# Optimization experiments

Measured on AMD Instinct MI355X. Metric: run time of the kernel, lower is better.

Reference implementation:

```python
import jax, jax.numpy as jnp
import numpy as np

N_NODES = 10000
N_EDGES = 160000
IN_DIM = 512
HID = 256
HEADS = 4
OUT_DIM = 512
NEG_SLOPE = 0.2  # PyG GATConv default


def _glorot(key, shape):
    fan_in, fan_out = shape[0], shape[-1]
    lim = jnp.sqrt(6.0 / (fan_in + fan_out))
    return jax.random.uniform(key, shape, jnp.float32, -lim, lim)


def setup_inputs() -> dict:
    key = jax.random.key(0)
    ks = jax.random.split(key, 16)
    x = jax.random.normal(ks[0], (N_NODES, IN_DIM), jnp.float32)
    edge_index = jax.random.randint(ks[1], (2, N_EDGES), 0, N_NODES, jnp.int64)
    # layer 1: GATConv(512 -> 256, heads=4, concat) -> out 1024
    W1 = _glorot(ks[2], (IN_DIM, HEADS * HID))
    att_src1 = _glorot(ks[3], (HEADS, HID))
    att_dst1 = _glorot(ks[4], (HEADS, HID))
    b1 = jnp.zeros((HEADS * HID,), jnp.float32)
    # layer 2: GATConv(1024 -> 256, heads=4, concat) -> out 1024
    W2 = _glorot(ks[5], (HEADS * HID, HEADS * HID))
    att_src2 = _glorot(ks[6], (HEADS, HID))
    att_dst2 = _glorot(ks[7], (HEADS, HID))
    b2 = jnp.zeros((HEADS * HID,), jnp.float32)
    # final fc: 1024 -> 512
    fcW = _glorot(ks[8], (HEADS * HID, OUT_DIM))
    fcb = jnp.zeros((OUT_DIM,), jnp.float32)
    return dict(x=x, edge_index=edge_index, W1=W1, att_src1=att_src1,
                att_dst1=att_dst1, b1=b1, W2=W2, att_src2=att_src2,
                att_dst2=att_dst2, b2=b2, fcW=fcW, fcb=fcb)


def gat_conv(x, src, dst, W, att_src, att_dst, bias):
    # x: [N, F_in]; src/dst: [E] (self-loops already included)
    N = x.shape[0]
    h = (x @ W).reshape(N, HEADS, HID)                       # [N, H, C]
    a_src = jnp.sum(h * att_src, axis=-1)                    # [N, H]
    a_dst = jnp.sum(h * att_dst, axis=-1)                    # [N, H]
    e = jax.nn.leaky_relu(a_src[src] + a_dst[dst], NEG_SLOPE)  # [E, H]
    # numerically stable segment softmax over destination nodes
    m = jax.ops.segment_max(e, dst, num_segments=N)          # [N, H]
    e = jnp.exp(e - m[dst])
    s = jax.ops.segment_sum(e, dst, num_segments=N)          # [N, H]
    alpha = e / (s[dst] + 1e-16)                             # [E, H]
    msg = alpha[:, :, None] * h[src]                         # [E, H, C]
    out = jax.ops.segment_sum(msg, dst, num_segments=N)      # [N, H, C]
    return out.reshape(N, HEADS * HID) + bias


def reference(x, edge_index, W1, att_src1, att_dst1, b1,
              W2, att_src2, att_dst2, b2, fcW, fcb):
    N = x.shape[0]
    loops = jnp.arange(N, dtype=edge_index.dtype)
    src = jnp.concatenate([edge_index[0], loops])  # PyG add_self_loops=True
    dst = jnp.concatenate([edge_index[1], loops])
    h = gat_conv(x, src, dst, W1, att_src1, att_dst1, b1)
    h = jax.nn.relu(h)  # dropout is identity in eval mode
    h = gat_conv(h, src, dst, W2, att_src2, att_dst2, b2)
    h = jax.nn.relu(h)
    return h @ fcW + fcb
```

## Files before the change

kernel.cpp:

```cpp
#include <hip/hip_runtime.h>
#include <hip/hip_bf16.h>

#define NN 10000
#define NE 160000
#define NET 170000
#define IN_DIM 512
#define D1 1024
#define HEADS 4
#define HID 256
#define OUT_DIM 512
#define NEG_SLOPE 0.2f

typedef __attribute__((ext_vector_type(8))) short bf16x8;
typedef __attribute__((ext_vector_type(4))) float f32x4;

__device__ inline float b2f(unsigned short b) {
    union { unsigned u; float f; } x; x.u = ((unsigned)b) << 16; return x.f;
}
__device__ inline unsigned short f2b(float f) {
    union { float f; unsigned u; } x; x.f = f;
    unsigned u = x.u;
    unsigned r = u + 0x7FFFu + ((u >> 16) & 1u);
    return (unsigned short)(r >> 16);
}
__device__ inline float lrelu(float v) { return v > 0.f ? v : NEG_SLOPE * v; }

__global__ void init_kernel(const int* ei32, int* flag, int* counts, int* cursor) {
    int i = blockIdx.x * blockDim.x + threadIdx.x;
    if (i < NN) { counts[i] = 0; cursor[i] = 0; }
    if (blockIdx.x == 0) {
        __shared__ int nz;
        if (threadIdx.x == 0) nz = 0;
        __syncthreads();
        int acc = 0;
        for (int k = threadIdx.x; k < 500; k += 256) acc |= ei32[2 * k + 1];
        if (acc) atomicOr(&nz, 1);
        __syncthreads();
        if (threadIdx.x == 0) flag[0] = (nz == 0) ? 1 : 0;
    }
}

__device__ inline void load_edge(const void* ei, int f64, int e, int& s, int& d) {
    if (f64) {
        const long long* p = (const long long*)ei;
        s = (int)p[e]; d = (int)p[NE + e];
    } else {
        const int* p = (const int*)ei;
        s = p[e]; d = p[NE + e];
    }
}

__global__ void count_kernel(const void* ei, const int* flag, int* counts) {
    int e = blockIdx.x * blockDim.x + threadIdx.x;
    if (e >= NET) return;
    int s, d;
    if (e < NE) load_edge(ei, *flag, e, s, d);
    else d = e - NE;
    atomicAdd(&counts[d], 1);
}

__global__ __launch_bounds__(256) void scan_kernel(const int* counts, int* indptr) {
    __shared__ int part[256];
    int t = threadIdx.x;
    int base = t * 40;
    int local[40];
    int sum = 0;
#pragma unroll
    for (int k = 0; k < 40; k++) {
        int i = base + k;
        int c = (i < NN) ? counts[i] : 0;
        local[k] = sum;
        sum += c;
    }
    part[t] = sum;
    __syncthreads();
    for (int off = 1; off < 256; off <<= 1) {
        int v = (t >= off) ? part[t - off] : 0;
        __syncthreads();
        part[t] += v;
        __syncthreads();
    }
    int excl = part[t] - sum;
#pragma unroll
    for (int k = 0; k < 40; k++) {
        int i = base + k;
        if (i < NN) indptr[i] = excl + local[k];
    }
    if (t == 255) indptr[NN] = part[255];
}

__global__ void fill_kernel(const void* ei, const int* flag, const int* indptr,
                            int* cursor, int* csr_src) {
    int e = blockIdx.x * blockDim.x + threadIdx.x;
    if (e >= NET) return;
    int s, d;
    if (e < NE) load_edge(ei, *flag, e, s, d);
    else { s = e - NE; d = s; }
    int pos = indptr[d] + atomicAdd(&cursor[d], 1);
    csr_src[pos] = s;
}

__device__ void tpose_tile(const float* __restrict__ in, unsigned short* __restrict__ out,
                           int R, int C, int bx, int by) {
    __shared__ float tile[32][33];
    int tx = threadIdx.x & 31, ty = threadIdx.x >> 5;
    int c = bx * 32 + tx;
#pragma unroll
    for (int r0 = 0; r0 < 32; r0 += 8) {
        int r = by * 32 + ty + r0;
        tile[ty + r0][tx] = in[(size_t)r * C + c];
    }
    __syncthreads();
    int oc = by * 32 + tx;
#pragma unroll
    for (int r0 = 0; r0 < 32; r0 += 8) {
        int orow = bx * 32 + ty + r0;
        out[(size_t)orow * R + oc] = f2b(tile[tx][ty + r0]);
    }
}

#define CVT_NB 5000
#define TP1_NB 512
#define TP2_NB 1024
#define TP3_NB 512
__global__ __launch_bounds__(256) void prep_kernel(
    const float* __restrict__ x, unsigned short* __restrict__ xb,
    const float* __restrict__ W1, unsigned short* __restrict__ W1t,
    const float* __restrict__ W2, unsigned short* __restrict__ W2t,
    const float* __restrict__ fcW, unsigned short* __restrict__ fcWt) {
    int b = blockIdx.x;
    if (b < CVT_NB) {
        int i = b * 256 + threadIdx.x;
        float4 v = reinterpret_cast<const float4*>(x)[i];
        ushort4 o;
        o.x = f2b(v.x); o.y = f2b(v.y); o.z = f2b(v.z); o.w = f2b(v.w);
        reinterpret_cast<ushort4*>(xb)[i] = o;
        return;
    }
    b -= CVT_NB;
    if (b < TP1_NB) { tpose_tile(W1, W1t, IN_DIM, D1, b & 31, b >> 5); return; }
    b -= TP1_NB;
    if (b < TP2_NB) { tpose_tile(W2, W2t, D1, D1, b & 31, b >> 5); return; }
    b -= TP2_NB;
    tpose_tile(fcW, fcWt, D1, OUT_DIM, b & 15, b >> 4);
}

#define BM 128
#define BN 128
#define BK 64
__global__ __launch_bounds__(256) void gemm128(
    const unsigned short* __restrict__ A, const unsigned short* __restrict__ B,
    const float* __restrict__ bias, float* __restrict__ Cf, unsigned short* __restrict__ Cb,
    int M, int N, int K, int NB) {
    __shared__ __align__(16) unsigned short As[BM * BK];
    __shared__ __align__(16) unsigned short Bs[BN * BK];
    int t = threadIdx.x;
    int nwg = gridDim.x;
    int q = nwg >> 3, r = nwg & 7;
    int xcd = blockIdx.x & 7, jj = blockIdx.x >> 3;
    int wg = (xcd < r ? xcd * (q + 1) : r * (q + 1) + (xcd - r) * q) + jj;
    int row0 = (wg / NB) * BM, col0 = (wg % NB) * BN;

    int w = t >> 6, l = t & 63;
    int wr = w >> 1, wc = w & 1;
    f32x4 acc[4][4] = {};

    int srow = w * 8 + (l >> 3);
    int scs = (((l & 7) ^ (l >> 3)) * 8);
    const unsigned short* ap0 = A + (size_t)min(row0 +  0 + srow, M - 1) * K + scs;
    const unsigned short* ap1 = A + (size_t)min(row0 + 32 + srow, M - 1) * K + scs;
    const unsigned short* ap2 = A + (size_t)min(row0 + 64 + srow, M - 1) * K + scs;
    const unsigned short* ap3 = A + (size_t)min(row0 + 96 + srow, M - 1) * K + scs;
    const unsigned short* bp0 = B + (size_t)(col0 +  0 + srow) * K + scs;
    const unsigned short* bp1 = B + (size_t)(col0 + 32 + srow) * K + scs;
    const unsigned short* bp2 = B + (size_t)(col0 + 64 + srow) * K + scs;
    const unsigned short* bp3 = B + (size_t)(col0 + 96 + srow) * K + scs;
    unsigned short* asd0 = As + 0 * 2048 + w * 512;
    unsigned short* asd1 = As + 1 * 2048 + w * 512;
    unsigned short* asd2 = As + 2 * 2048 + w * 512;
    unsigned short* asd3 = As + 3 * 2048 + w * 512;
    unsigned short* bsd0 = Bs + 0 * 2048 + w * 512;
    unsigned short* bsd1 = Bs + 1 * 2048 + w * 512;
    unsigned short* bsd2 = Bs + 2 * 2048 + w * 512;
    unsigned short* bsd3 = Bs + 3 * 2048 + w * 512;

    int rr = l & 15;
    int rb = (rr & 7) << 4;
    int kb0 = (l >> 4) << 4;
    const char* Ab = (const char*)As;
    const char* Bb = (const char*)Bs;

#define GLD(src, dst) __builtin_amdgcn_global_load_lds( \
        (const __attribute__((address_space(1))) void*)(src), \
        (__attribute__((address_space(3))) void*)(dst), 16, 0, 0)

    for (int k0 = 0; k0 < K; k0 += BK) {
        GLD(ap0, asd0); GLD(ap1, asd1); GLD(ap2, asd2); GLD(ap3, asd3);
        GLD(bp0, bsd0); GLD(bp1, bsd1); GLD(bp2, bsd2); GLD(bp3, bsd3);
        ap0 += BK; ap1 += BK; ap2 += BK; ap3 += BK;
        bp0 += BK; bp1 += BK; bp2 += BK; bp3 += BK;
        __syncthreads();

#pragma unroll
        for (int ks = 0; ks < 2; ks++) {
            int kb = ((ks << 6) | kb0) ^ rb;
            bf16x8 af[4], bfv[4];
#pragma unroll
            for (int mi = 0; mi < 4; mi++)
                af[mi] = *reinterpret_cast<const bf16x8*>(
                    Ab + (wr * 64 + mi * 16 + rr) * 128 + kb);
#pragma unroll
            for (int ni = 0; ni < 4; ni++)
                bfv[ni] = *reinterpret_cast<const bf16x8*>(
                    Bb + (wc * 64 + ni * 16 + rr) * 128 + kb);
#pragma unroll
            for (int mi = 0; mi < 4; mi++)
#pragma unroll
                for (int ni = 0; ni < 4; ni++)
                    acc[mi][ni] = __builtin_amdgcn_mfma_f32_16x16x32_bf16(
                        af[mi], bfv[ni], acc[mi][ni], 0, 0, 0);
        }
        __syncthreads();
    }
#undef GLD

    int c_l = l & 15, r_h = (l >> 4) * 4;
#pragma unroll
    for (int mi = 0; mi < 4; mi++)
#pragma unroll
        for (int ni = 0; ni < 4; ni++) {
            int gc = col0 + wc * 64 + ni * 16 + c_l;
#pragma unroll
            for (int j = 0; j < 4; j++) {
                int gr = row0 + wr * 64 + mi * 16 + r_h + j;
                if (gr < M) {
                    float v = acc[mi][ni][j];
                    if (bias) v += bias[gc];
                    if (Cf) Cf[(size_t)gr * N + gc] = v;
                    if (Cb) Cb[(size_t)gr * N + gc] = f2b(v);
                }
            }
        }
}

__global__ __launch_bounds__(256) void att_kernel(const unsigned short* __restrict__ hb,
                                                  const float* __restrict__ att_s,
                                                  const float* __restrict__ att_d,
                                                  float* __restrict__ aS, float* __restrict__ aD) {
    int node = blockIdx.x * 4 + (threadIdx.x >> 6);
    int l = threadIdx.x & 63;
    int head = l >> 4, qq = l & 15;
    const unsigned short* hrow = hb + (size_t)node * D1 + head * HID + qq * 16;
    bf16x8 h0 = *reinterpret_cast<const bf16x8*>(hrow);
    bf16x8 h1 = *reinterpret_cast<const bf16x8*>(hrow + 8);
    const float* asp = att_s + head * HID + qq * 16;
    const float* adp = att_d + head * HID + qq * 16;
    float ps = 0.f, pd = 0.f;
#pragma unroll
    for (int c = 0; c < 8; c++) {
        float hv = b2f((unsigned short)h0[c]);
        float hw = b2f((unsigned short)h1[c]);
        ps += hv * asp[c] + hw * asp[8 + c];
        pd += hv * adp[c] + hw * adp[8 + c];
    }
#pragma unroll
    for (int off = 1; off <= 8; off <<= 1) {
        ps += __shfl_xor(ps, off);
        pd += __shfl_xor(pd, off);
    }
    if (qq == 0) {
        aS[node * HEADS + head] = ps;
        aD[node * HEADS + head] = pd;
    }
}

__global__ __launch_bounds__(256) void alpha_kernel(
    const float* __restrict__ aS, const float* __restrict__ aD,
    const int* __restrict__ indptr, const int* __restrict__ csr_src,
    float* __restrict__ alpha, float* __restrict__ einv) {
    int node = blockIdx.x * 4 + (threadIdx.x >> 6);
    int l = threadIdx.x & 63;
    int beg = indptr[node], deg = indptr[node + 1] - beg;
    float4 ad = *reinterpret_cast<const float4*>(aD + node * HEADS);
    float s0 = 0.f, s1 = 0.f, s2 = 0.f, s3 = 0.f;
    for (int j = l; j < deg; j += 64) {
        int s = csr_src[beg + j];
        float4 a = *reinterpret_cast<const float4*>(aS + s * HEADS);
        float e0 = __expf(lrelu(a.x + ad.x));
        float e1 = __expf(lrelu(a.y + ad.y));
        float e2 = __expf(lrelu(a.z + ad.z));
        float e3 = __expf(lrelu(a.w + ad.w));
        alpha[0 * NET + beg + j] = e0;
        alpha[1 * NET + beg + j] = e1;
        alpha[2 * NET + beg + j] = e2;
        alpha[3 * NET + beg + j] = e3;
        s0 += e0; s1 += e1; s2 += e2; s3 += e3;
    }
#pragma unroll
    for (int off = 32; off; off >>= 1) {
        s0 += __shfl_xor(s0, off);
        s1 += __shfl_xor(s1, off);
        s2 += __shfl_xor(s2, off);
        s3 += __shfl_xor(s3, off);
    }
    if (l == 0) {
        float4 iv;
        iv.x = 1.f / (s0 + 1e-16f);
        iv.y = 1.f / (s1 + 1e-16f);
        iv.z = 1.f / (s2 + 1e-16f);
        iv.w = 1.f / (s3 + 1e-16f);
        *reinterpret_cast<float4*>(einv + node * HEADS) = iv;
    }
}

__global__ __launch_bounds__(256) void agg_kernel(const unsigned short* __restrict__ hb,
                                                  const float* __restrict__ alpha,
                                                  const float* __restrict__ einv,
                                                  const int* __restrict__ indptr,
                                                  const int* __restrict__ csr_src,
                                                  const float* __restrict__ bias,
                                                  unsigned short* __restrict__ outb) {
    int slice = blockIdx.x & 7;
    int node = __builtin_amdgcn_readfirstlane((blockIdx.x >> 3) * 4 + (threadIdx.x >> 6));
    int l = threadIdx.x & 63;
    int head = slice >> 1;
    int cbase = slice * 128 + l * 2;
    int beg = indptr[node];
    int deg = indptr[node + 1] - beg;
    const int* cs = csr_src + beg;
    const float* ap = alpha + head * NET + beg;
    const unsigned short* hp = hb + cbase;
    float acc0 = 0.f, acc1 = 0.f;
    int dm = deg - 1;
    for (int j = 0; j < deg; j += 8) {
        int i1 = min(j + 1, dm), i2 = min(j + 2, dm), i3 = min(j + 3, dm);
        int i4 = min(j + 4, dm), i5 = min(j + 5, dm), i6 = min(j + 6, dm), i7 = min(j + 7, dm);
        int s0 = cs[j],  s1 = cs[i1], s2 = cs[i2], s3 = cs[i3];
        int s4 = cs[i4], s5 = cs[i5], s6 = cs[i6], s7 = cs[i7];
        float a0 = ap[j];
        float a1 = (j + 1 <= dm) ? ap[i1] : 0.f;
        float a2 = (j + 2 <= dm) ? ap[i2] : 0.f;
        float a3 = (j + 3 <= dm) ? ap[i3] : 0.f;
        float a4 = (j + 4 <= dm) ? ap[i4] : 0.f;
        float a5 = (j + 5 <= dm) ? ap[i5] : 0.f;
        float a6 = (j + 6 <= dm) ? ap[i6] : 0.f;
        float a7 = (j + 7 <= dm) ? ap[i7] : 0.f;
        unsigned r0 = *reinterpret_cast<const unsigned*>(hp + (size_t)s0 * D1);
        unsigned r1 = *reinterpret_cast<const unsigned*>(hp + (size_t)s1 * D1);
        unsigned r2 = *reinterpret_cast<const unsigned*>(hp + (size_t)s2 * D1);
        unsigned r3 = *reinterpret_cast<const unsigned*>(hp + (size_t)s3 * D1);
        unsigned r4 = *reinterpret_cast<const unsigned*>(hp + (size_t)s4 * D1);
        unsigned r5 = *reinterpret_cast<const unsigned*>(hp + (size_t)s5 * D1);
        unsigned r6 = *reinterpret_cast<const unsigned*>(hp + (size_t)s6 * D1);
        unsigned r7 = *reinterpret_cast<const unsigned*>(hp + (size_t)s7 * D1);
        acc0 += a0 * b2f((unsigned short)(r0 & 0xFFFF)) + a1 * b2f((unsigned short)(r1 & 0xFFFF))
              + a2 * b2f((unsigned short)(r2 & 0xFFFF)) + a3 * b2f((unsigned short)(r3 & 0xFFFF))
              + a4 * b2f((unsigned short)(r4 & 0xFFFF)) + a5 * b2f((unsigned short)(r5 & 0xFFFF))
              + a6 * b2f((unsigned short)(r6 & 0xFFFF)) + a7 * b2f((unsigned short)(r7 & 0xFFFF));
        acc1 += a0 * b2f((unsigned short)(r0 >> 16)) + a1 * b2f((unsigned short)(r1 >> 16))
              + a2 * b2f((unsigned short)(r2 >> 16)) + a3 * b2f((unsigned short)(r3 >> 16))
              + a4 * b2f((unsigned short)(r4 >> 16)) + a5 * b2f((unsigned short)(r5 >> 16))
              + a6 * b2f((unsigned short)(r6 >> 16)) + a7 * b2f((unsigned short)(r7 >> 16));
    }
    float inv = einv[node * HEADS + head];
    ushort2 o;
    o.x = f2b(fmaxf(acc0 * inv + bias[cbase], 0.f));
    o.y = f2b(fmaxf(acc1 * inv + bias[cbase + 1], 0.f));
    *reinterpret_cast<ushort2*>(outb + (size_t)node * D1 + cbase) = o;
}

extern "C" void kernel_launch(void* const* d_in, const int* in_sizes, int n_in,
                              void* d_out, int out_size, void* d_ws, size_t ws_size,
                              hipStream_t stream) {
    const float* x   = (const float*)d_in[0];
    const void*  ei  = d_in[1];
    const float* W1  = (const float*)d_in[2];
    const float* as1 = (const float*)d_in[3];
    const float* ad1 = (const float*)d_in[4];
    const float* b1  = (const float*)d_in[5];
    const float* W2  = (const float*)d_in[6];
    const float* as2 = (const float*)d_in[7];
    const float* ad2 = (const float*)d_in[8];
    const float* b2  = (const float*)d_in[9];
    const float* fcW = (const float*)d_in[10];
    const float* fcb = (const float*)d_in[11];
    float* out = (float*)d_out;

    char* ws = (char*)d_ws;
    size_t o = 0;
    auto carve = [&](size_t bytes) -> char* {
        char* p = ws + o;
        o = (o + bytes + 255) & ~(size_t)255;
        return p;
    };
    unsigned short* xb   = (unsigned short*)carve((size_t)NN * IN_DIM * 2);
    unsigned short* hb   = (unsigned short*)carve((size_t)NN * D1 * 2);
    unsigned short* x2b  = (unsigned short*)carve((size_t)NN * D1 * 2);
    unsigned short* W1t  = (unsigned short*)carve((size_t)D1 * IN_DIM * 2);
    unsigned short* W2t  = (unsigned short*)carve((size_t)D1 * D1 * 2);
    unsigned short* fcWt = (unsigned short*)carve((size_t)OUT_DIM * D1 * 2);
    float* aS    = (float*)carve((size_t)NN * HEADS * 4);
    float* aD    = (float*)carve((size_t)NN * HEADS * 4);
    float* alpha = (float*)carve((size_t)NET * HEADS * 4);
    float* einv  = (float*)carve((size_t)NN * HEADS * 4);
    int* counts = (int*)carve((size_t)NN * 4);
    int* cursor = (int*)carve((size_t)NN * 4);
    int* indptr = (int*)carve((size_t)(NN + 1) * 4);
    int* csr_src= (int*)carve((size_t)NET * 4);
    int* flag   = (int*)carve(4);
    (void)ws_size; (void)in_sizes; (void)n_in; (void)out_size;

    init_kernel<<<(NN + 255) / 256, 256, 0, stream>>>((const int*)ei, flag, counts, cursor);
    count_kernel<<<(NET + 255) / 256, 256, 0, stream>>>(ei, flag, counts);
    scan_kernel<<<1, 256, 0, stream>>>(counts, indptr);
    fill_kernel<<<(NET + 255) / 256, 256, 0, stream>>>(ei, flag, indptr, cursor, csr_src);

    prep_kernel<<<CVT_NB + TP1_NB + TP2_NB + TP3_NB, 256, 0, stream>>>(
        x, xb, W1, W1t, W2, W2t, fcW, fcWt);

    const int MB = (NN + BM - 1) / BM;
    gemm128<<<MB * (D1 / BN), 256, 0, stream>>>(xb, W1t, nullptr, nullptr, hb,
                                                NN, D1, IN_DIM, D1 / BN);
    att_kernel<<<NN / 4, 256, 0, stream>>>(hb, as1, ad1, aS, aD);
    alpha_kernel<<<NN / 4, 256, 0, stream>>>(aS, aD, indptr, csr_src, alpha, einv);
    agg_kernel<<<(NN / 4) * 8, 256, 0, stream>>>(hb, alpha, einv, indptr, csr_src, b1, x2b);
    gemm128<<<MB * (D1 / BN), 256, 0, stream>>>(x2b, W2t, nullptr, nullptr, hb,
                                                NN, D1, D1, D1 / BN);
    att_kernel<<<NN / 4, 256, 0, stream>>>(hb, as2, ad2, aS, aD);
    alpha_kernel<<<NN / 4, 256, 0, stream>>>(aS, aD, indptr, csr_src, alpha, einv);
    agg_kernel<<<(NN / 4) * 8, 256, 0, stream>>>(hb, alpha, einv, indptr, csr_src, b2, x2b);
    gemm128<<<MB * (OUT_DIM / BN), 256, 0, stream>>>(x2b, fcWt, fcb, out, nullptr,
                                                     NN, OUT_DIM, D1, OUT_DIM / BN);
}
```

Measured before the change: 279.6 us.

## Pad CSR rows to multiples of eight and vectorize aggregation gathers

Each node's CSR segment is padded to a multiple of 8 edges, with padded slots pointing at node 0 and carrying zero weight. The aggregation kernel can then read indices and weights as aligned int4/float4 without bounds clamping. Each wave now splits its 64 lanes into 4 edge groups of 16 lanes, each lane loading 8 bf16 channels at once, and combines the groups with cross-lane shuffles. The aim is fewer, wider memory requests per gathered row. The cost is extra padded-edge work, larger alpha and csr buffers, and a zero-fill of csr_src inside init.

```diff
diff --git a/kernel.cpp b/kernel.cpp
--- a/kernel.cpp
+++ b/kernel.cpp
@@ -4,6 +4,7 @@
 #define NN 10000
 #define NE 160000
 #define NET 170000
+#define CAPE 250048
 #define IN_DIM 512
 #define D1 1024
 #define HEADS 4
@@ -25,9 +26,11 @@
 }
 __device__ inline float lrelu(float v) { return v > 0.f ? v : NEG_SLOPE * v; }
 
-__global__ void init_kernel(const int* ei32, int* flag, int* counts, int* cursor) {
+__global__ void init_kernel(const int* ei32, int* flag, int* counts, int* cursor,
+                            int* csr_src) {
     int i = blockIdx.x * blockDim.x + threadIdx.x;
     if (i < NN) { counts[i] = 0; cursor[i] = 0; }
+    for (int k = i; k < CAPE; k += 40 * 256) csr_src[k] = 0;
     if (blockIdx.x == 0) {
         __shared__ int nz;
         if (threadIdx.x == 0) nz = 0;
@@ -68,7 +71,7 @@
 #pragma unroll
     for (int k = 0; k < 40; k++) {
         int i = base + k;
-        int c = (i < NN) ? counts[i] : 0;
+        int c = (i < NN) ? ((counts[i] + 7) & ~7) : 0;
         local[k] = sum;
         sum += c;
     }
@@ -276,24 +279,28 @@
 
 __global__ __launch_bounds__(256) void alpha_kernel(
     const float* __restrict__ aS, const float* __restrict__ aD,
-    const int* __restrict__ indptr, const int* __restrict__ csr_src,
+    const int* __restrict__ indptr, const int* __restrict__ counts,
+    const int* __restrict__ csr_src,
     float* __restrict__ alpha, float* __restrict__ einv) {
     int node = blockIdx.x * 4 + (threadIdx.x >> 6);
     int l = threadIdx.x & 63;
-    int beg = indptr[node], deg = indptr[node + 1] - beg;
+    int beg = indptr[node];
+    int pdeg = indptr[node + 1] - beg;
+    int rdeg = counts[node];
     float4 ad = *reinterpret_cast<const float4*>(aD + node * HEADS);
     float s0 = 0.f, s1 = 0.f, s2 = 0.f, s3 = 0.f;
-    for (int j = l; j < deg; j += 64) {
+    for (int j = l; j < pdeg; j += 64) {
         int s = csr_src[beg + j];
         float4 a = *reinterpret_cast<const float4*>(aS + s * HEADS);
-        float e0 = __expf(lrelu(a.x + ad.x));
-        float e1 = __expf(lrelu(a.y + ad.y));
-        float e2 = __expf(lrelu(a.z + ad.z));
-        float e3 = __expf(lrelu(a.w + ad.w));
-        alpha[0 * NET + beg + j] = e0;
-        alpha[1 * NET + beg + j] = e1;
-        alpha[2 * NET + beg + j] = e2;
-        alpha[3 * NET + beg + j] = e3;
+        bool real = j < rdeg;
+        float e0 = real ? __expf(lrelu(a.x + ad.x)) : 0.f;
+        float e1 = real ? __expf(lrelu(a.y + ad.y)) : 0.f;
+        float e2 = real ? __expf(lrelu(a.z + ad.z)) : 0.f;
+        float e3 = real ? __expf(lrelu(a.w + ad.w)) : 0.f;
+        alpha[0 * CAPE + beg + j] = e0;
+        alpha[1 * CAPE + beg + j] = e1;
+        alpha[2 * CAPE + beg + j] = e2;
+        alpha[3 * CAPE + beg + j] = e3;
         s0 += e0; s1 += e1; s2 += e2; s3 += e3;
     }
 #pragma unroll
@@ -321,52 +328,61 @@
                                                   const float* __restrict__ bias,
                                                   unsigned short* __restrict__ outb) {
     int slice = blockIdx.x & 7;
-    int node = __builtin_amdgcn_readfirstlane((blockIdx.x >> 3) * 4 + (threadIdx.x >> 6));
+    int node = (blockIdx.x >> 3) * 4 + (threadIdx.x >> 6);
     int l = threadIdx.x & 63;
+    int q = l >> 4;
+    int c = l & 15;
     int head = slice >> 1;
-    int cbase = slice * 128 + l * 2;
+    int cbase = slice * 128 + c * 8;
     int beg = indptr[node];
-    int deg = indptr[node + 1] - beg;
+    int pdeg = indptr[node + 1] - beg;
     const int* cs = csr_src + beg;
-    const float* ap = alpha + head * NET + beg;
+    const float* ap = alpha + head * CAPE + beg;
     const unsigned short* hp = hb + cbase;
-    float acc0 = 0.f, acc1 = 0.f;
-    int dm = deg - 1;
-    for (int j = 0; j < deg; j += 8) {
-        int i1 = min(j + 1, dm), i2 = min(j + 2, dm), i3 = min(j + 3, dm);
-        int i4 = min(j + 4, dm), i5 = min(j + 5, dm), i6 = min(j + 6, dm), i7 = min(j + 7, dm);
-        int s0 = cs[j],  s1 = cs[i1], s2 = cs[i2], s3 = cs[i3];
-        int s4 = cs[i4], s5 = cs[i5], s6 = cs[i6], s7 = cs[i7];
-        float a0 = ap[j];
-        float a1 = (j + 1 <= dm) ? ap[i1] : 0.f;
-        float a2 = (j + 2 <= dm) ? ap[i2] : 0.f;
-        float a3 = (j + 3 <= dm) ? ap[i3] : 0.f;
-        float a4 = (j + 4 <= dm) ? ap[i4] : 0.f;
-        float a5 = (j + 5 <= dm) ? ap[i5] : 0.f;
-        float a6 = (j + 6 <= dm) ? ap[i6] : 0.f;
-        float a7 = (j + 7 <= dm) ? ap[i7] : 0.f;
-        unsigned r0 = *reinterpret_cast<const unsigned*>(hp + (size_t)s0 * D1);
-        unsigned r1 = *reinterpret_cast<const unsigned*>(hp + (size_t)s1 * D1);
-        unsigned r2 = *reinterpret_cast<const unsigned*>(hp + (size_t)s2 * D1);
-        unsigned r3 = *reinterpret_cast<const unsigned*>(hp + (size_t)s3 * D1);
-        unsigned r4 = *reinterpret_cast<const unsigned*>(hp + (size_t)s4 * D1);
-        unsigned r5 = *reinterpret_cast<const unsigned*>(hp + (size_t)s5 * D1);
-        unsigned r6 = *reinterpret_cast<const unsigned*>(hp + (size_t)s6 * D1);
-        unsigned r7 = *reinterpret_cast<const unsigned*>(hp + (size_t)s7 * D1);
-        acc0 += a0 * b2f((unsigned short)(r0 & 0xFFFF)) + a1 * b2f((unsigned short)(r1 & 0xFFFF))
-              + a2 * b2f((unsigned short)(r2 & 0xFFFF)) + a3 * b2f((unsigned short)(r3 & 0xFFFF))
-              + a4 * b2f((unsigned short)(r4 & 0xFFFF)) + a5 * b2f((unsigned short)(r5 & 0xFFFF))
-              + a6 * b2f((unsigned short)(r6 & 0xFFFF)) + a7 * b2f((unsigned short)(r7 & 0xFFFF));
-        acc1 += a0 * b2f((unsigned short)(r0 >> 16)) + a1 * b2f((unsigned short)(r1 >> 16))
-              + a2 * b2f((unsigned short)(r2 >> 16)) + a3 * b2f((unsigned short)(r3 >> 16))
-              + a4 * b2f((unsigned short)(r4 >> 16)) + a5 * b2f((unsigned short)(r5 >> 16))
-              + a6 * b2f((unsigned short)(r6 >> 16)) + a7 * b2f((unsigned short)(r7 >> 16));
-    }
-    float inv = einv[node * HEADS + head];
-    ushort2 o;
-    o.x = f2b(fmaxf(acc0 * inv + bias[cbase], 0.f));
-    o.y = f2b(fmaxf(acc1 * inv + bias[cbase + 1], 0.f));
-    *reinterpret_cast<ushort2*>(outb + (size_t)node * D1 + cbase) = o;
+    float a0 = 0.f, a1 = 0.f, a2 = 0.f, a3 = 0.f;
+    float a4 = 0.f, a5 = 0.f, a6 = 0.f, a7 = 0.f;
+    for (int j = 0; j < pdeg; j += 8) {
+        int4 sA = *reinterpret_cast<const int4*>(cs + j);
+        int4 sB = *reinterpret_cast<const int4*>(cs + j + 4);
+        float4 wA = *reinterpret_cast<const float4*>(ap + j);
+        float4 wB = *reinterpret_cast<const float4*>(ap + j + 4);
+        int sa = (q & 2) ? ((q & 1) ? sA.w : sA.z) : ((q & 1) ? sA.y : sA.x);
+        int sb = (q & 2) ? ((q & 1) ? sB.w : sB.z) : ((q & 1) ? sB.y : sB.x);
+        float wa = (q & 2) ? ((q & 1) ? wA.w : wA.z) : ((q & 1) ? wA.y : wA.x);
+        float wb = (q & 2) ? ((q & 1) ? wB.w : wB.z) : ((q & 1) ? wB.y : wB.x);
+        bf16x8 va = *reinterpret_cast<const bf16x8*>(hp + (size_t)sa * D1);
+        bf16x8 vb = *reinterpret_cast<const bf16x8*>(hp + (size_t)sb * D1);
+        a0 += wa * b2f((unsigned short)va[0]) + wb * b2f((unsigned short)vb[0]);
+        a1 += wa * b2f((unsigned short)va[1]) + wb * b2f((unsigned short)vb[1]);
+        a2 += wa * b2f((unsigned short)va[2]) + wb * b2f((unsigned short)vb[2]);
+        a3 += wa * b2f((unsigned short)va[3]) + wb * b2f((unsigned short)vb[3]);
+        a4 += wa * b2f((unsigned short)va[4]) + wb * b2f((unsigned short)vb[4]);
+        a5 += wa * b2f((unsigned short)va[5]) + wb * b2f((unsigned short)vb[5]);
+        a6 += wa * b2f((unsigned short)va[6]) + wb * b2f((unsigned short)vb[6]);
+        a7 += wa * b2f((unsigned short)va[7]) + wb * b2f((unsigned short)vb[7]);
+    }
+#pragma unroll
+    for (int off = 16; off <= 32; off <<= 1) {
+        a0 += __shfl_xor(a0, off); a1 += __shfl_xor(a1, off);
+        a2 += __shfl_xor(a2, off); a3 += __shfl_xor(a3, off);
+        a4 += __shfl_xor(a4, off); a5 += __shfl_xor(a5, off);
+        a6 += __shfl_xor(a6, off); a7 += __shfl_xor(a7, off);
+    }
+    if (q == 0) {
+        float inv = einv[node * HEADS + head];
+        float4 b0 = *reinterpret_cast<const float4*>(bias + cbase);
+        float4 b1 = *reinterpret_cast<const float4*>(bias + cbase + 4);
+        bf16x8 o;
+        o[0] = (short)f2b(fmaxf(a0 * inv + b0.x, 0.f));
+        o[1] = (short)f2b(fmaxf(a1 * inv + b0.y, 0.f));
+        o[2] = (short)f2b(fmaxf(a2 * inv + b0.z, 0.f));
+        o[3] = (short)f2b(fmaxf(a3 * inv + b0.w, 0.f));
+        o[4] = (short)f2b(fmaxf(a4 * inv + b1.x, 0.f));
+        o[5] = (short)f2b(fmaxf(a5 * inv + b1.y, 0.f));
+        o[6] = (short)f2b(fmaxf(a6 * inv + b1.z, 0.f));
+        o[7] = (short)f2b(fmaxf(a7 * inv + b1.w, 0.f));
+        *reinterpret_cast<bf16x8*>(outb + (size_t)node * D1 + cbase) = o;
+    }
 }
 
 extern "C" void kernel_launch(void* const* d_in, const int* in_sizes, int n_in,
@@ -401,16 +417,16 @@
     unsigned short* fcWt = (unsigned short*)carve((size_t)OUT_DIM * D1 * 2);
     float* aS    = (float*)carve((size_t)NN * HEADS * 4);
     float* aD    = (float*)carve((size_t)NN * HEADS * 4);
-    float* alpha = (float*)carve((size_t)NET * HEADS * 4);
+    float* alpha = (float*)carve((size_t)CAPE * HEADS * 4);
     float* einv  = (float*)carve((size_t)NN * HEADS * 4);
     int* counts = (int*)carve((size_t)NN * 4);
     int* cursor = (int*)carve((size_t)NN * 4);
     int* indptr = (int*)carve((size_t)(NN + 1) * 4);
-    int* csr_src= (int*)carve((size_t)NET * 4);
+    int* csr_src= (int*)carve((size_t)CAPE * 4);
     int* flag   = (int*)carve(4);
     (void)ws_size; (void)in_sizes; (void)n_in; (void)out_size;
 
-    init_kernel<<<(NN + 255) / 256, 256, 0, stream>>>((const int*)ei, flag, counts, cursor);
+    init_kernel<<<(NN + 255) / 256, 256, 0, stream>>>((const int*)ei, flag, counts, cursor, csr_src);
     count_kernel<<<(NET + 255) / 256, 256, 0, stream>>>(ei, flag, counts);
     scan_kernel<<<1, 256, 0, stream>>>(counts, indptr);
     fill_kernel<<<(NET + 255) / 256, 256, 0, stream>>>(ei, flag, indptr, cursor, csr_src);
@@ -422,12 +438,12 @@
     gemm128<<<MB * (D1 / BN), 256, 0, stream>>>(xb, W1t, nullptr, nullptr, hb,
                                                 NN, D1, IN_DIM, D1 / BN);
     att_kernel<<<NN / 4, 256, 0, stream>>>(hb, as1, ad1, aS, aD);
-    alpha_kernel<<<NN / 4, 256, 0, stream>>>(aS, aD, indptr, csr_src, alpha, einv);
+    alpha_kernel<<<NN / 4, 256, 0, stream>>>(aS, aD, indptr, counts, csr_src, alpha, einv);
     agg_kernel<<<(NN / 4) * 8, 256, 0, stream>>>(hb, alpha, einv, indptr, csr_src, b1, x2b);
     gemm128<<<MB * (D1 / BN), 256, 0, stream>>>(x2b, W2t, nullptr, nullptr, hb,
                                                 NN, D1, D1, D1 / BN);
     att_kernel<<<NN / 4, 256, 0, stream>>>(hb, as2, ad2, aS, aD);
-    alpha_kernel<<<NN / 4, 256, 0, stream>>>(aS, aD, indptr, csr_src, alpha, einv);
+    alpha_kernel<<<NN / 4, 256, 0, stream>>>(aS, aD, indptr, counts, csr_src, alpha, einv);
     agg_kernel<<<(NN / 4) * 8, 256, 0, stream>>>(hb, alpha, einv, indptr, csr_src, b2, x2b);
     gemm128<<<MB * (OUT_DIM / BN), 256, 0, stream>>>(x2b, fcWt, fcb, out, nullptr,
                                                      NN, OUT_DIM, D1, OUT_DIM / BN);
```

Measured after the change: 295.1 us. 5.5% more time.
